# Kernel optimization log

Measured on AMD Instinct MI355X. Metric: run time of the kernel, lower is better.

## Reference

```python
import jax, jax.numpy as jnp
import numpy as np

NW, NT, ND, D = 30000, 2000, 20000, 128
E = {'ww': 600000, 'wt': 300000, 'wd': 400000, 'td': 100000, 'tt': 40000}
ENDS = {'ww': (NW, NW), 'wt': (NW, NT), 'wd': (NW, ND), 'td': (NT, ND), 'tt': (NT, NT)}


def setup_inputs() -> dict:
    key = jax.random.key(0)
    ks = iter(jax.random.split(key, 64))
    nrm = lambda shape: jax.random.normal(next(ks), shape, dtype=jnp.float32)
    inp = {}
    inp['feat_word'] = nrm((NW, D))
    inp['feat_topic'] = nrm((NT, D))
    # 'effect' node data: ~half the topics are causal (nonzero effect)
    inp['effect'] = jax.random.randint(next(ks), (NT,), 0, 2).astype(jnp.float32)
    # independent Bernoulli(0.1) draws for the td and tt iterations
    inp['bern_td'] = (jax.random.uniform(next(ks), (NT,)) < 0.1).astype(jnp.float32)
    inp['bern_tt'] = (jax.random.uniform(next(ks), (NT,)) < 0.1).astype(jnp.float32)
    for et, (ns, nd) in ENDS.items():
        inp[f'src_{et}'] = jax.random.randint(next(ks), (E[et],), 0, ns, dtype=jnp.int32)
        inp[f'dst_{et}'] = jax.random.randint(next(ks), (E[et],), 0, nd, dtype=jnp.int32)
        inp[f'w_{et}'] = jax.random.uniform(next(ks), (E[et],), dtype=jnp.float32)
    for name in ['ww', 'wt', 'wd', 'td', 'tt']:
        inp[f'W_{name}'] = nrm((D, D)) * 0.05
        inp[f'b_{name}'] = jnp.zeros((D,), jnp.float32)
    inp['W_causal'] = nrm((D, D)) * 0.05
    inp['W_noise'] = nrm((D, D)) * 0.05
    inp['n_doc'] = ND
    return inp


def _mean_agg(Wh, w, src, dst, n_dst):
    # DGL fn.u_mul_e + fn.mean: mean of (Wh[src]*w) over incoming edges; 0 for isolated dst
    m = Wh[src] * w[:, None]                                    # [E, D]
    s = jax.ops.segment_sum(m, dst, num_segments=n_dst)          # [n_dst, D]
    deg = jax.ops.segment_sum(jnp.ones_like(w), dst, num_segments=n_dst)
    return jnp.where(deg[:, None] > 0, s / jnp.maximum(deg, 1.0)[:, None], 0.0)


def reference(feat_word, feat_topic, effect, bern_td, bern_tt,
              src_ww, dst_ww, w_ww, src_wt, dst_wt, w_wt,
              src_wd, dst_wd, w_wd, src_td, dst_td, w_td,
              src_tt, dst_tt, w_tt,
              W_ww, b_ww, W_wt, b_wt, W_wd, b_wd, W_td, b_td, W_tt, b_tt,
              W_causal, W_noise, n_doc):
    n_word, n_topic = feat_word.shape[0], feat_topic.shape[0]
    # Phase 1: word -> word (ww)
    h_word = _mean_agg(feat_word @ W_ww + b_ww, w_ww, src_ww, dst_ww, n_word)
    # Phase 2: remaining etypes; word features replaced by h
    causal = (effect != 0).astype(feat_topic.dtype)[:, None]     # [NT, 1]
    rm_td = (bern_td * (effect == 0))[:, None]
    rm_tt = (bern_tt * (effect == 0))[:, None]
    Wh_wt = h_word @ W_wt + b_wt
    Wh_wd = h_word @ W_wd + b_wd
    Wh_td = (feat_topic @ W_td + b_td
             + (feat_topic * causal) @ W_causal - (feat_topic * rm_td) @ W_noise)
    Wh_tt = (feat_topic @ W_tt + b_tt
             + (feat_topic * causal) @ W_causal - (feat_topic * rm_tt) @ W_noise)
    # cross-relation 'sum' reducer per destination ntype
    h_topic = (_mean_agg(Wh_wt, w_wt, src_wt, dst_wt, n_topic)
               + _mean_agg(Wh_tt, w_tt, src_tt, dst_tt, n_topic))
    h_doc = (_mean_agg(Wh_wd, w_wd, src_wd, dst_wd, n_doc)
             + _mean_agg(Wh_td, w_td, src_td, dst_td, n_doc))
    return h_word, h_topic, h_doc
```

## Files before the change

### kernel.cpp

```cpp
#include <hip/hip_runtime.h>

#define D 128
typedef unsigned short u16;
constexpr int NW = 30000;
constexpr int NT = 2000;
constexpr int NDOC = 20000;

constexpr int CAPB = 1024;
constexpr int SSP  = 136;
constexpr int NBK_WW = (NW + 31) / 32;
constexpr int NBK_WT = NT / 4;
constexpr int NBK_TT = (NT + 31) / 32;
constexpr int NBK_WD = (NDOC + 31) / 32;
constexpr int NBK_TD = (NDOC + 31) / 32;
constexpr int BUK_WW = 0;
constexpr int BUK_WT = BUK_WW + NBK_WW;
constexpr int BUK_TT = BUK_WT + NBK_WT;
constexpr int BUK_WD = BUK_TT + NBK_TT;
constexpr int BUK_TD = BUK_WD + NBK_WD;
constexpr int NBUK   = BUK_TD + NBK_TD;

constexpr int EPB  = 4096;
constexpr int NF2B = (NW * D / 4 + 255) / 256;
constexpr int NMM4C = 32 * 4;
constexpr int NWTR  = 3 * 4;
constexpr int U3 = NBK_WW + NBK_TT + NBK_TD;
constexpr int U4 = NBK_WT + NBK_WD;

struct RelDesc { const int* src; const int* dst; const float* w;
                 int e0; int buk0; int shift; int mask; };
struct Rels { RelDesc r[5]; };

__device__ __forceinline__ int which_rel(const Rels& R, int e)
{
    if (e < R.r[1].e0) return 0;
    if (e < R.r[2].e0) return 1;
    if (e < R.r[3].e0) return 2;
    if (e < R.r[4].e0) return 3;
    return 4;
}

__device__ __forceinline__ float b2f(u16 h)
{
    return __uint_as_float(((unsigned)h) << 16);
}
__device__ __forceinline__ u16 f2b(float f)
{
    unsigned u = __float_as_uint(f);
    return (u16)((u + 0x7FFF + ((u >> 16) & 1)) >> 16);
}

typedef short bf16x8 __attribute__((ext_vector_type(8)));
typedef float f32x4 __attribute__((ext_vector_type(4)));
constexpr int WPITCH = 136;

struct BucketSmem {
    int2 st[CAPB];
    u16  Ssum[32 * SSP];
    float degL[32];
    float wsumL[32];
    int h2[32], exc[32], cnt[32];
};
struct PartSm { int hist[NBUK]; int baseL[NBUK]; };
union K1Sm {
    PartSm pt;
    u16 Wts[32 * WPITCH];
};

struct FP {
    const float *feat_word, *feat_topic;
    const float *effect, *bern_td, *bern_tt;
    Rels R;
    int Etot, npb;
    const float *W_td, *W_tt, *W_c, *W_n;
    const float *W_ww, *W_wt, *W_wd;
    const float *b_ww, *b_wt, *b_wd, *b_td, *b_tt;
    int* cur; int2* edataP;
    u16 *fw16, *hw16, *wtd16, *wtt16;
    u16 *Wtg_ww, *Wtg_wt, *Wtg_wd;
    u16* Sb2; float* degf2;
    float *h_word, *h_topic, *h_doc;
};

__device__ __forceinline__ void mm_slice(
    const float* __restrict__ Wg, int cs, u16* Wts, int tid)
{
    for (int i = tid; i < 32 * D; i += 256) {
        int k = i >> 5, nl = i & 31;
        Wts[nl * WPITCH + k] = f2b(Wg[k * D + cs * 32 + nl]);
    }
}

__device__ __forceinline__ void mm_acc2(
    const bf16x8 a[4], const u16* Wts, int lanelo, int quad, f32x4 acc[2])
{
#pragma unroll
    for (int c = 0; c < 2; ++c) {
        acc[c][0] = 0.f; acc[c][1] = 0.f; acc[c][2] = 0.f; acc[c][3] = 0.f;
    }
#pragma unroll
    for (int k0 = 0; k0 < 4; ++k0) {
#pragma unroll
        for (int c = 0; c < 2; ++c) {
            bf16x8 b = *(const bf16x8*)&Wts[(c * 16 + lanelo) * WPITCH
                                            + k0 * 32 + quad * 8];
            acc[c] = __builtin_amdgcn_mfma_f32_16x16x32_bf16(a[k0], b, acc[c], 0, 0, 0);
        }
    }
}

__device__ __forceinline__ void reduce_one_lds(
    const u16* __restrict__ Xb, const int2* st,
    int start, int end, int dl, int lane, BucketSmem& s)
{
    int half = lane >> 5;
    int q = (lane & 31) * 4;
    float4 acc = make_float4(0.f, 0.f, 0.f, 0.f);
    float wacc = 0.f;
    int j = start;
    for (; j + 32 <= end; j += 32) {
        int2 ee[16];
        ushort4 vv[16];
#pragma unroll
        for (int t = 0; t < 16; ++t) ee[t] = st[j + 2 * t + half];
#pragma unroll
        for (int t = 0; t < 16; ++t)
            vv[t] = *(const ushort4*)(Xb + (size_t)(ee[t].x & 0x7FFF) * D + q);
#pragma unroll
        for (int t = 0; t < 16; ++t) {
            float w = __int_as_float(ee[t].y);
            acc.x = fmaf(w, b2f(vv[t].x), acc.x);
            acc.y = fmaf(w, b2f(vv[t].y), acc.y);
            acc.z = fmaf(w, b2f(vv[t].z), acc.z);
            acc.w = fmaf(w, b2f(vv[t].w), acc.w);
            wacc += w;
        }
    }
    if (j + 16 <= end) {
        int2 ee[8];
        ushort4 vv[8];
#pragma unroll
        for (int t = 0; t < 8; ++t) ee[t] = st[j + 2 * t + half];
#pragma unroll
        for (int t = 0; t < 8; ++t)
            vv[t] = *(const ushort4*)(Xb + (size_t)(ee[t].x & 0x7FFF) * D + q);
#pragma unroll
        for (int t = 0; t < 8; ++t) {
            float w = __int_as_float(ee[t].y);
            acc.x = fmaf(w, b2f(vv[t].x), acc.x);
            acc.y = fmaf(w, b2f(vv[t].y), acc.y);
            acc.z = fmaf(w, b2f(vv[t].z), acc.z);
            acc.w = fmaf(w, b2f(vv[t].w), acc.w);
            wacc += w;
        }
        j += 16;
    }
    if (j + 8 <= end) {
        int2 ee[4];
        ushort4 vv[4];
#pragma unroll
        for (int t = 0; t < 4; ++t) ee[t] = st[j + 2 * t + half];
#pragma unroll
        for (int t = 0; t < 4; ++t)
            vv[t] = *(const ushort4*)(Xb + (size_t)(ee[t].x & 0x7FFF) * D + q);
#pragma unroll
        for (int t = 0; t < 4; ++t) {
            float w = __int_as_float(ee[t].y);
            acc.x = fmaf(w, b2f(vv[t].x), acc.x);
            acc.y = fmaf(w, b2f(vv[t].y), acc.y);
            acc.z = fmaf(w, b2f(vv[t].z), acc.z);
            acc.w = fmaf(w, b2f(vv[t].w), acc.w);
            wacc += w;
        }
        j += 8;
    }
    if (j + 4 <= end) {
        int2 ea = st[j + half];
        int2 eb = st[j + 2 + half];
        ushort4 va = *(const ushort4*)(Xb + (size_t)(ea.x & 0x7FFF) * D + q);
        ushort4 vb = *(const ushort4*)(Xb + (size_t)(eb.x & 0x7FFF) * D + q);
        float wa = __int_as_float(ea.y);
        float wb = __int_as_float(eb.y);
        acc.x = fmaf(wa, b2f(va.x), acc.x); acc.y = fmaf(wa, b2f(va.y), acc.y);
        acc.z = fmaf(wa, b2f(va.z), acc.z); acc.w = fmaf(wa, b2f(va.w), acc.w);
        acc.x = fmaf(wb, b2f(vb.x), acc.x); acc.y = fmaf(wb, b2f(vb.y), acc.y);
        acc.z = fmaf(wb, b2f(vb.z), acc.z); acc.w = fmaf(wb, b2f(vb.w), acc.w);
        wacc += wa + wb;
        j += 4;
    }
    for (; j < end; j += 2) {
        int jj = j + half;
        int2 e = st[jj < end ? jj : (end - 1)];
        float w = (jj < end) ? __int_as_float(e.y) : 0.f;
        ushort4 v = *(const ushort4*)(Xb + (size_t)(e.x & 0x7FFF) * D + q);
        acc.x = fmaf(w, b2f(v.x), acc.x); acc.y = fmaf(w, b2f(v.y), acc.y);
        acc.z = fmaf(w, b2f(v.z), acc.z); acc.w = fmaf(w, b2f(v.w), acc.w);
        wacc += w;
    }
    acc.x += __shfl_xor(acc.x, 32);
    acc.y += __shfl_xor(acc.y, 32);
    acc.z += __shfl_xor(acc.z, 32);
    acc.w += __shfl_xor(acc.w, 32);
    wacc  += __shfl_xor(wacc, 32);
    if (half == 0) {
        ushort4 o;
        o.x = f2b(acc.x); o.y = f2b(acc.y); o.z = f2b(acc.z); o.w = f2b(acc.w);
        *(ushort4*)(s.Ssum + dl * SSP + q) = o;
    }
    if (lane == 0) {
        s.degL[dl] = (float)(end - start);
        s.wsumL[dl] = wacc;
    }
}

__device__ __forceinline__ void bucket_reduce(
    const u16* __restrict__ X, const int* __restrict__ cur,
    const int2* __restrict__ edataP, int buk, int nsl, BucketSmem& s)
{
    int tid = threadIdx.x;
    int nE = min(cur[buk], CAPB);
    const int2* gsrc = edataP + (size_t)buk * CAPB;
    int2 ev[CAPB / 256];
#pragma unroll
    for (int t = 0; t < CAPB / 256; ++t) {
        int i = t * 256 + tid;
        if (i < nE) ev[t] = gsrc[i];
    }
    if (tid < 32) { s.h2[tid] = 0; s.cnt[tid] = 0; }
    __syncthreads();
#pragma unroll
    for (int t = 0; t < CAPB / 256; ++t) {
        int i = t * 256 + tid;
        if (i < nE) atomicAdd(&s.h2[(ev[t].x >> 15) & 31], 1);
    }
    __syncthreads();
    if (tid < 32) s.exc[tid] = s.h2[tid];
    __syncthreads();
    for (int off = 1; off < 32; off <<= 1) {
        int t = 0;
        if (tid < 32 && tid >= off) t = s.exc[tid - off];
        __syncthreads();
        if (tid < 32) s.exc[tid] += t;
        __syncthreads();
    }
    if (tid < 32) s.exc[tid] -= s.h2[tid];
    __syncthreads();
#pragma unroll
    for (int t = 0; t < CAPB / 256; ++t) {
        int i = t * 256 + tid;
        if (i < nE) {
            int dl = (ev[t].x >> 15) & 31;
            int rk = atomicAdd(&s.cnt[dl], 1);
            s.st[s.exc[dl] + rk] = ev[t];
        }
    }
    __syncthreads();
    int wv = tid >> 6, lane = tid & 63;
    for (int dl = wv; dl < nsl; dl += 4) {
        int start = s.exc[dl];
        reduce_one_lds(X, s.st, start, start + s.h2[dl], dl, lane, s);
    }
}

__device__ __forceinline__ void fused_mm(
    BucketSmem& s, const u16* __restrict__ Wtg, const float* __restrict__ bias,
    const u16* __restrict__ Tg, const float* __restrict__ degTg,
    float* __restrict__ Y, u16* __restrict__ Yb, int row0, int n, int tid)
{
    int wv = tid >> 6, lane = tid & 63;
    int lanelo = lane & 15, quad = lane >> 4;
    int rt = wv >> 1, ch = wv & 1;
    int arow = rt * 16 + lanelo;
    f32x4 acc[4];
#pragma unroll
    for (int c = 0; c < 4; ++c) {
        acc[c][0] = 0.f; acc[c][1] = 0.f; acc[c][2] = 0.f; acc[c][3] = 0.f;
    }
#pragma unroll
    for (int k0 = 0; k0 < 4; ++k0) {
        bf16x8 a;
        if (arow < n) {
            a = *(const bf16x8*)(s.Ssum + arow * SSP + k0 * 32 + quad * 8);
        } else {
#pragma unroll
            for (int j = 0; j < 8; ++j) a[j] = 0;
        }
#pragma unroll
        for (int c = 0; c < 4; ++c) {
            int ct = ch * 4 + c;
            bf16x8 b = *(const bf16x8*)(Wtg + (ct * 16 + lanelo) * D
                                        + k0 * 32 + quad * 8);
            acc[c] = __builtin_amdgcn_mfma_f32_16x16x32_bf16(a, b, acc[c], 0, 0, 0);
        }
    }
    int rbase = rt * 16 + quad * 4;
#pragma unroll
    for (int r = 0; r < 4; ++r) {
        int row = rbase + r;
        if (row >= n) continue;
        float dgv = s.degL[row];
        float wsv = s.wsumL[row];
        float dtv = degTg ? degTg[row] : 0.f;
#pragma unroll
        for (int c = 0; c < 4; ++c) {
            int ct = ch * 4 + c;
            int col = ct * 16 + lanelo;
            float y = acc[c][r];
            y = dgv > 0.f ? (y + wsv * bias[col]) / dgv : 0.f;
            if (Tg && dtv > 0.f) y += b2f(Tg[(size_t)row * D + col]) / dtv;
            Y[(size_t)(row0 + row) * D + col] = y;
            if (Yb) Yb[(size_t)(row0 + row) * D + col] = f2b(y);
        }
    }
}

__device__ __forceinline__ void dump_smem(
    BucketSmem& s, u16* __restrict__ Sg, float* __restrict__ degg,
    int nsl, int tid)
{
    for (int i = tid; i < nsl * 32; i += 256) {
        int row = i >> 5, c4 = (i & 31) * 4;
        *(ushort4*)(Sg + (size_t)row * D + c4) =
            *(const ushort4*)(s.Ssum + row * SSP + c4);
    }
    if (tid < nsl) degg[tid] = s.degL[tid];
}

__global__ __launch_bounds__(256) void prep_part_kernel(FP p)
{
    __shared__ K1Sm sm;
    int tid = threadIdx.x;
    int u = (int)blockIdx.x;

    if (u < p.npb) {
        for (int i = tid; i < NBUK; i += 256) sm.pt.hist[i] = 0;
        __syncthreads();
        int base_e = u * EPB;
        int bs[EPB / 256];
        int2 se[EPB / 256];
#pragma unroll
        for (int r = 0; r < EPB / 256; ++r) {
            int e = base_e + r * 256 + tid;
            if (e < p.Etot) {
                int k = which_rel(p.R, e);
                int le = e - p.R.r[k].e0;
                int s = p.R.r[k].src[le];
                int dd = p.R.r[k].dst[le];
                float w = p.R.r[k].w[le];
                int b = p.R.r[k].buk0 + (dd >> p.R.r[k].shift);
                int dloc = dd & p.R.r[k].mask;
                bs[r] = b;
                se[r] = make_int2(s | (dloc << 15), __float_as_int(w));
                atomicAdd(&sm.pt.hist[b], 1);
            } else {
                bs[r] = -1;
            }
        }
        __syncthreads();
        for (int i = tid; i < NBUK; i += 256)
            sm.pt.baseL[i] = sm.pt.hist[i]
                ? atomicAdd(&p.cur[i], sm.pt.hist[i]) : 0;
        __syncthreads();
        for (int i = tid; i < NBUK; i += 256) sm.pt.hist[i] = 0;
        __syncthreads();
#pragma unroll
        for (int r = 0; r < EPB / 256; ++r) {
            int b = bs[r];
            if (b >= 0) {
                int rk = atomicAdd(&sm.pt.hist[b], 1) + sm.pt.baseL[b];
                if (rk < CAPB)
                    p.edataP[(size_t)b * CAPB + rk] = se[r];
            }
        }
    } else if (u < p.npb + NF2B) {
        int i = (u - p.npb) * 256 + tid;
        if (i < NW * D / 4) {
            float4 v = ((const float4*)p.feat_word)[i];
            ushort4 o;
            o.x = f2b(v.x); o.y = f2b(v.y); o.z = f2b(v.z); o.w = f2b(v.w);
            ((ushort4*)p.fw16)[i] = o;
        }
    } else if (u < p.npb + NF2B + NMM4C) {
        int idx = u - p.npb - NF2B;
        int rt = idx >> 2, cs = idx & 3;
        int wv = tid >> 6, lane = tid & 63;
        int lanelo = lane & 15, quad = lane >> 4;
        int arow = rt * 64 + wv * 16 + lanelo;
        bf16x8 a[4];
#pragma unroll
        for (int k0 = 0; k0 < 4; ++k0) {
            if (arow < NT) {
                const float* ap = p.feat_topic + (size_t)arow * D
                                  + k0 * 32 + quad * 8;
                float4 a0 = *(const float4*)ap;
                float4 a1 = *(const float4*)(ap + 4);
                a[k0][0] = (short)f2b(a0.x); a[k0][1] = (short)f2b(a0.y);
                a[k0][2] = (short)f2b(a0.z); a[k0][3] = (short)f2b(a0.w);
                a[k0][4] = (short)f2b(a1.x); a[k0][5] = (short)f2b(a1.y);
                a[k0][6] = (short)f2b(a1.z); a[k0][7] = (short)f2b(a1.w);
            } else {
#pragma unroll
                for (int j = 0; j < 8; ++j) a[k0][j] = 0;
            }
        }
        f32x4 aC[2], aN[2], aM[2];
        mm_slice(p.W_c, cs, sm.Wts, tid);  __syncthreads();
        mm_acc2(a, sm.Wts, lanelo, quad, aC); __syncthreads();
        mm_slice(p.W_n, cs, sm.Wts, tid);  __syncthreads();
        mm_acc2(a, sm.Wts, lanelo, quad, aN); __syncthreads();

        int rbase = rt * 64 + wv * 16 + quad * 4;
#pragma unroll
        for (int m = 0; m < 2; ++m) {
            const float* Wg   = m == 0 ? p.W_td : p.W_tt;
            const float* bias = m == 0 ? p.b_td : p.b_tt;
            const float* bern = m == 0 ? p.bern_td : p.bern_tt;
            u16* out = m == 0 ? p.wtd16 : p.wtt16;
            mm_slice(Wg, cs, sm.Wts, tid); __syncthreads();
            mm_acc2(a, sm.Wts, lanelo, quad, aM);
            float b0 = bias[cs * 32 + lanelo];
            float b1 = bias[cs * 32 + 16 + lanelo];
#pragma unroll
            for (int r = 0; r < 4; ++r) {
                int row = rbase + r;
                if (row >= NT) continue;
                float eff = p.effect[row];
                float causal = (eff != 0.f) ? 1.f : 0.f;
                float zero = (eff == 0.f) ? 1.f : 0.f;
                float rm = bern[row] * zero;
                float v0 = aM[0][r] + b0 + causal * aC[0][r] - rm * aN[0][r];
                float v1 = aM[1][r] + b1 + causal * aC[1][r] - rm * aN[1][r];
                out[(size_t)row * D + cs * 32 + lanelo] = f2b(v0);
                out[(size_t)row * D + cs * 32 + 16 + lanelo] = f2b(v1);
            }
            __syncthreads();
        }
    } else {
        int idx = u - p.npb - NF2B - NMM4C;
        int which = idx >> 2, cs = idx & 3;
        const float* Wg = which == 0 ? p.W_ww : which == 1 ? p.W_wt : p.W_wd;
        u16* Wd = which == 0 ? p.Wtg_ww : which == 1 ? p.Wtg_wt : p.Wtg_wd;
        mm_slice(Wg, cs, sm.Wts, tid);
        __syncthreads();
        for (int i = tid; i < 32 * D; i += 256) {
            int nl = i >> 7, k = i & 127;
            Wd[(size_t)(cs * 32 + nl) * D + k] = sm.Wts[nl * WPITCH + k];
        }
    }
}

__global__ __launch_bounds__(256, 4) void phaseA_kernel(FP p)
{
    __shared__ BucketSmem bs;
    int u = (int)blockIdx.x;
    int tid = threadIdx.x;
    if (u < NBK_WW) {
        int w0 = u * 32;
        int nsl = min(32, NW - w0);
        bucket_reduce(p.fw16, p.cur, p.edataP, BUK_WW + u, nsl, bs);
        __syncthreads();
        fused_mm(bs, p.Wtg_ww, p.b_ww, nullptr, nullptr,
                 p.h_word, p.hw16, w0, nsl, tid);
    } else if (u < NBK_WW + NBK_TT) {
        int i = u - NBK_WW;
        int t0 = i * 32;
        int nsl = min(32, NT - t0);
        bucket_reduce(p.wtt16, p.cur, p.edataP, BUK_TT + i, nsl, bs);
        __syncthreads();
        dump_smem(bs, p.Sb2 + (size_t)t0 * D, p.degf2 + t0, nsl, tid);
    } else {
        int i = u - NBK_WW - NBK_TT;
        int d0 = i * 32;
        int nsl = min(32, NDOC - d0);
        bucket_reduce(p.wtd16, p.cur, p.edataP, BUK_TD + i, nsl, bs);
        __syncthreads();
        dump_smem(bs, p.Sb2 + (size_t)(NT + d0) * D, p.degf2 + NT + d0, nsl, tid);
    }
}

__global__ __launch_bounds__(256, 4) void phaseB_kernel(FP p)
{
    __shared__ BucketSmem bs;
    int u = (int)blockIdx.x;
    int tid = threadIdx.x;
    if (u < NBK_WT) {
        int t0 = u * 4;
        bucket_reduce(p.hw16, p.cur, p.edataP, BUK_WT + u, 4, bs);
        __syncthreads();
        fused_mm(bs, p.Wtg_wt, p.b_wt, p.Sb2 + (size_t)t0 * D,
                 p.degf2 + t0, p.h_topic, nullptr, t0, 4, tid);
    } else {
        int i = u - NBK_WT;
        int d0 = i * 32;
        int nsl = min(32, NDOC - d0);
        bucket_reduce(p.hw16, p.cur, p.edataP, BUK_WD + i, nsl, bs);
        __syncthreads();
        fused_mm(bs, p.Wtg_wd, p.b_wd, p.Sb2 + (size_t)(NT + d0) * D,
                 p.degf2 + NT + d0, p.h_doc, nullptr, d0, nsl, tid);
    }
}

extern "C" void kernel_launch(void* const* d_in, const int* in_sizes, int n_in,
                              void* d_out, int out_size, void* d_ws, size_t ws_size,
                              hipStream_t stream)
{
    const float* feat_word  = (const float*)d_in[0];
    const float* feat_topic = (const float*)d_in[1];
    const float* effect     = (const float*)d_in[2];
    const float* bern_td    = (const float*)d_in[3];
    const float* bern_tt    = (const float*)d_in[4];
    const int*   src_ww = (const int*)d_in[5];
    const int*   dst_ww = (const int*)d_in[6];
    const float* w_ww   = (const float*)d_in[7];
    const int*   src_wt = (const int*)d_in[8];
    const int*   dst_wt = (const int*)d_in[9];
    const float* w_wt   = (const float*)d_in[10];
    const int*   src_wd = (const int*)d_in[11];
    const int*   dst_wd = (const int*)d_in[12];
    const float* w_wd   = (const float*)d_in[13];
    const int*   src_td = (const int*)d_in[14];
    const int*   dst_td = (const int*)d_in[15];
    const float* w_td   = (const float*)d_in[16];
    const int*   src_tt = (const int*)d_in[17];
    const int*   dst_tt = (const int*)d_in[18];
    const float* w_tt   = (const float*)d_in[19];
    const float* W_ww = (const float*)d_in[20];
    const float* b_ww = (const float*)d_in[21];
    const float* W_wt = (const float*)d_in[22];
    const float* b_wt = (const float*)d_in[23];
    const float* W_wd = (const float*)d_in[24];
    const float* b_wd = (const float*)d_in[25];
    const float* W_td = (const float*)d_in[26];
    const float* b_td = (const float*)d_in[27];
    const float* W_tt = (const float*)d_in[28];
    const float* b_tt = (const float*)d_in[29];
    const float* W_causal = (const float*)d_in[30];
    const float* W_noise  = (const float*)d_in[31];

    const int E_ww = in_sizes[5];
    const int E_wt = in_sizes[8];
    const int E_wd = in_sizes[11];
    const int E_td = in_sizes[14];
    const int E_tt = in_sizes[17];
    const int E_total = E_ww + E_wt + E_wd + E_td + E_tt;

    float* ws = (float*)d_ws;
    u16*   Sb2   = (u16*)ws; ws += (long long)(NT + NDOC) * D / 2;
    float* degf2 = ws; ws += NT + NDOC;
    int*   cur   = (int*)ws; ws += NBUK;
    ws += ((size_t)(ws - (float*)d_ws) & 1);
    int2*  edataP = (int2*)ws; ws += (long long)2 * NBUK * CAPB;
    u16*   fw16  = (u16*)ws;  ws += (long long)NW * D / 2;
    u16*   hw16  = (u16*)ws;  ws += (long long)NW * D / 2;
    u16*   wtd16 = (u16*)ws;  ws += (long long)NT * D / 2;
    u16*   wtt16 = (u16*)ws;  ws += (long long)NT * D / 2;
    u16*   Wtg_ww = (u16*)ws; ws += (long long)D * D / 2;
    u16*   Wtg_wt = (u16*)ws; ws += (long long)D * D / 2;
    u16*   Wtg_wd = (u16*)ws; ws += (long long)D * D / 2;

    float* h_word  = (float*)d_out;
    float* h_topic = h_word + (long long)NW * D;
    float* h_doc   = h_topic + (long long)NT * D;

    FP p;
    p.feat_word = feat_word; p.feat_topic = feat_topic;
    p.effect = effect; p.bern_td = bern_td; p.bern_tt = bern_tt;
    p.R.r[0] = { src_ww, dst_ww, w_ww, 0,                         BUK_WW, 5, 31 };
    p.R.r[1] = { src_wt, dst_wt, w_wt, E_ww,                      BUK_WT, 2, 3  };
    p.R.r[2] = { src_tt, dst_tt, w_tt, E_ww + E_wt,               BUK_TT, 5, 31 };
    p.R.r[3] = { src_wd, dst_wd, w_wd, E_ww + E_wt + E_tt,        BUK_WD, 5, 31 };
    p.R.r[4] = { src_td, dst_td, w_td, E_ww + E_wt + E_tt + E_wd, BUK_TD, 5, 31 };
    p.Etot = E_total;
    p.npb = (E_total + EPB - 1) / EPB;
    p.W_td = W_td; p.W_tt = W_tt; p.W_c = W_causal; p.W_n = W_noise;
    p.W_ww = W_ww; p.W_wt = W_wt; p.W_wd = W_wd;
    p.b_ww = b_ww; p.b_wt = b_wt; p.b_wd = b_wd; p.b_td = b_td; p.b_tt = b_tt;
    p.cur = cur; p.edataP = edataP;
    p.fw16 = fw16; p.hw16 = hw16; p.wtd16 = wtd16; p.wtt16 = wtt16;
    p.Wtg_ww = Wtg_ww; p.Wtg_wt = Wtg_wt; p.Wtg_wd = Wtg_wd;
    p.Sb2 = Sb2; p.degf2 = degf2;
    p.h_word = h_word; p.h_topic = h_topic; p.h_doc = h_doc;

    hipMemsetAsync(cur, 0, NBUK * sizeof(int), stream);

    unsigned g1 = (unsigned)(p.npb + NF2B + NMM4C + NWTR);
    prep_part_kernel<<<g1, 256, 0, stream>>>(p);

    phaseA_kernel<<<U3, 256, 0, stream>>>(p);

    phaseB_kernel<<<U4, 256, 0, stream>>>(p);

    (void)n_in; (void)in_sizes; (void)out_size; (void)ws_size;
}
```

Baseline: 246.2 us.

## Split each destination bucket across two blocks handling half the rows

Each 32-destination bucket is now processed by two blocks, each reducing and multiplying only 16 destination rows, with the block index remapped so both halves of a bucket run in adjacent groups of 8. Shared memory for the partial sums shrinks to 16 rows and the fused MFMA matmul is reshaped so each wave handles two 16-column tiles of a single 16-row tile. The goal is more blocks and smaller per-block LDS, giving more parallelism and occupancy across the GPU. The cost is that both blocks load, histogram and sort the full bucket edge list, duplicating that work.

```diff
diff --git a/kernel.cpp b/kernel.cpp
--- a/kernel.cpp
+++ b/kernel.cpp
@@ -26,6 +26,8 @@
 constexpr int NWTR  = 3 * 4;
 constexpr int U3 = NBK_WW + NBK_TT + NBK_TD;
 constexpr int U4 = NBK_WT + NBK_WD;
+constexpr int GA = ((U3 + 7) / 8) * 16;
+constexpr int GB = ((U4 + 7) / 8) * 16;
 
 struct RelDesc { const int* src; const int* dst; const float* w;
                  int e0; int buk0; int shift; int mask; };
@@ -56,9 +58,9 @@
 
 struct BucketSmem {
     int2 st[CAPB];
-    u16  Ssum[32 * SSP];
-    float degL[32];
-    float wsumL[32];
+    u16  Ssum[16 * SSP];
+    float degL[16];
+    float wsumL[16];
     int h2[32], exc[32], cnt[32];
 };
 struct PartSm { int hist[NBUK]; int baseL[NBUK]; };
@@ -213,9 +215,9 @@
     }
 }
 
-__device__ __forceinline__ void bucket_reduce(
+__device__ __forceinline__ void bucket_reduce_half(
     const u16* __restrict__ X, const int* __restrict__ cur,
-    const int2* __restrict__ edataP, int buk, int nsl, BucketSmem& s)
+    const int2* __restrict__ edataP, int buk, int dl0, int nslh, BucketSmem& s)
 {
     int tid = threadIdx.x;
     int nE = min(cur[buk], CAPB);
@@ -256,44 +258,43 @@
     }
     __syncthreads();
     int wv = tid >> 6, lane = tid & 63;
-    for (int dl = wv; dl < nsl; dl += 4) {
+    for (int dll = wv; dll < nslh; dll += 4) {
+        int dl = dl0 + dll;
         int start = s.exc[dl];
-        reduce_one_lds(X, s.st, start, start + s.h2[dl], dl, lane, s);
-    }
-}
-
-__device__ __forceinline__ void fused_mm(
+        reduce_one_lds(X, s.st, start, start + s.h2[dl], dll, lane, s);
+    }
+}
+
+__device__ __forceinline__ void fused_mm16(
     BucketSmem& s, const u16* __restrict__ Wtg, const float* __restrict__ bias,
     const u16* __restrict__ Tg, const float* __restrict__ degTg,
-    float* __restrict__ Y, u16* __restrict__ Yb, int row0, int n, int tid)
+    float* __restrict__ Y, u16* __restrict__ Yb, long long row0, int n, int tid)
 {
     int wv = tid >> 6, lane = tid & 63;
     int lanelo = lane & 15, quad = lane >> 4;
-    int rt = wv >> 1, ch = wv & 1;
-    int arow = rt * 16 + lanelo;
-    f32x4 acc[4];
-#pragma unroll
-    for (int c = 0; c < 4; ++c) {
+    f32x4 acc[2];
+#pragma unroll
+    for (int c = 0; c < 2; ++c) {
         acc[c][0] = 0.f; acc[c][1] = 0.f; acc[c][2] = 0.f; acc[c][3] = 0.f;
     }
 #pragma unroll
     for (int k0 = 0; k0 < 4; ++k0) {
         bf16x8 a;
-        if (arow < n) {
-            a = *(const bf16x8*)(s.Ssum + arow * SSP + k0 * 32 + quad * 8);
+        if (lanelo < n) {
+            a = *(const bf16x8*)(s.Ssum + lanelo * SSP + k0 * 32 + quad * 8);
         } else {
 #pragma unroll
             for (int j = 0; j < 8; ++j) a[j] = 0;
         }
 #pragma unroll
-        for (int c = 0; c < 4; ++c) {
-            int ct = ch * 4 + c;
+        for (int c = 0; c < 2; ++c) {
+            int ct = wv * 2 + c;
             bf16x8 b = *(const bf16x8*)(Wtg + (ct * 16 + lanelo) * D
                                         + k0 * 32 + quad * 8);
             acc[c] = __builtin_amdgcn_mfma_f32_16x16x32_bf16(a, b, acc[c], 0, 0, 0);
         }
     }
-    int rbase = rt * 16 + quad * 4;
+    int rbase = quad * 4;
 #pragma unroll
     for (int r = 0; r < 4; ++r) {
         int row = rbase + r;
@@ -302,19 +303,19 @@
         float wsv = s.wsumL[row];
         float dtv = degTg ? degTg[row] : 0.f;
 #pragma unroll
-        for (int c = 0; c < 4; ++c) {
-            int ct = ch * 4 + c;
+        for (int c = 0; c < 2; ++c) {
+            int ct = wv * 2 + c;
             int col = ct * 16 + lanelo;
             float y = acc[c][r];
             y = dgv > 0.f ? (y + wsv * bias[col]) / dgv : 0.f;
             if (Tg && dtv > 0.f) y += b2f(Tg[(size_t)row * D + col]) / dtv;
-            Y[(size_t)(row0 + row) * D + col] = y;
-            if (Yb) Yb[(size_t)(row0 + row) * D + col] = f2b(y);
-        }
-    }
-}
-
-__device__ __forceinline__ void dump_smem(
+            Y[(row0 + row) * D + col] = y;
+            if (Yb) Yb[(row0 + row) * D + col] = f2b(y);
+        }
+    }
+}
+
+__device__ __forceinline__ void dump_smem16(
     BucketSmem& s, u16* __restrict__ Sg, float* __restrict__ degg,
     int nsl, int tid)
 {
@@ -452,51 +453,60 @@
 __global__ __launch_bounds__(256, 4) void phaseA_kernel(FP p)
 {
     __shared__ BucketSmem bs;
-    int u = (int)blockIdx.x;
+    int b = (int)blockIdx.x;
+    int u = ((b >> 4) << 3) | (b & 7);
+    int h = (b >> 3) & 1;
     int tid = threadIdx.x;
+    if (u >= U3) return;
     if (u < NBK_WW) {
-        int w0 = u * 32;
-        int nsl = min(32, NW - w0);
-        bucket_reduce(p.fw16, p.cur, p.edataP, BUK_WW + u, nsl, bs);
-        __syncthreads();
-        fused_mm(bs, p.Wtg_ww, p.b_ww, nullptr, nullptr,
-                 p.h_word, p.hw16, w0, nsl, tid);
+        long long w0 = (long long)u * 32 + h * 16;
+        int nslh = min(16, NW - (int)w0);
+        if (nslh <= 0) return;
+        bucket_reduce_half(p.fw16, p.cur, p.edataP, BUK_WW + u, h * 16, nslh, bs);
+        __syncthreads();
+        fused_mm16(bs, p.Wtg_ww, p.b_ww, nullptr, nullptr,
+                   p.h_word, p.hw16, w0, nslh, tid);
     } else if (u < NBK_WW + NBK_TT) {
         int i = u - NBK_WW;
-        int t0 = i * 32;
-        int nsl = min(32, NT - t0);
-        bucket_reduce(p.wtt16, p.cur, p.edataP, BUK_TT + i, nsl, bs);
-        __syncthreads();
-        dump_smem(bs, p.Sb2 + (size_t)t0 * D, p.degf2 + t0, nsl, tid);
+        int t0 = i * 32 + h * 16;
+        int nslh = min(16, NT - t0);
+        if (nslh <= 0) return;
+        bucket_reduce_half(p.wtt16, p.cur, p.edataP, BUK_TT + i, h * 16, nslh, bs);
+        __syncthreads();
+        dump_smem16(bs, p.Sb2 + (size_t)t0 * D, p.degf2 + t0, nslh, tid);
     } else {
         int i = u - NBK_WW - NBK_TT;
-        int d0 = i * 32;
-        int nsl = min(32, NDOC - d0);
-        bucket_reduce(p.wtd16, p.cur, p.edataP, BUK_TD + i, nsl, bs);
-        __syncthreads();
-        dump_smem(bs, p.Sb2 + (size_t)(NT + d0) * D, p.degf2 + NT + d0, nsl, tid);
+        int d0 = i * 32 + h * 16;
+        int nslh = min(16, NDOC - d0);
+        if (nslh <= 0) return;
+        bucket_reduce_half(p.wtd16, p.cur, p.edataP, BUK_TD + i, h * 16, nslh, bs);
+        __syncthreads();
+        dump_smem16(bs, p.Sb2 + (size_t)(NT + d0) * D, p.degf2 + NT + d0,
+                    nslh, tid);
     }
 }
 
 __global__ __launch_bounds__(256, 4) void phaseB_kernel(FP p)
 {
     __shared__ BucketSmem bs;
-    int u = (int)blockIdx.x;
+    int b = (int)blockIdx.x;
+    int u = ((b >> 4) << 3) | (b & 7);
+    int h = (b >> 3) & 1;
     int tid = threadIdx.x;
+    if (u >= U4) return;
     if (u < NBK_WT) {
-        int t0 = u * 4;
-        bucket_reduce(p.hw16, p.cur, p.edataP, BUK_WT + u, 4, bs);
-        __syncthreads();
-        fused_mm(bs, p.Wtg_wt, p.b_wt, p.Sb2 + (size_t)t0 * D,
-                 p.degf2 + t0, p.h_topic, nullptr, t0, 4, tid);
+        int t0 = u * 4 + h * 2;
+        bucket_reduce_half(p.hw16, p.cur, p.edataP, BUK_WT + u, h * 2, 2, bs);
+        __syncthreads();
+        fused_mm16(bs, p.Wtg_wt, p.b_wt, p.Sb2 + (size_t)t0 * D,
+                   p.degf2 + t0, p.h_topic, nullptr, t0, 2, tid);
     } else {
         int i = u - NBK_WT;
-        int d0 = i * 32;
-        int nsl = min(32, NDOC - d0);
-        bucket_reduce(p.hw16, p.cur, p.edataP, BUK_WD + i, nsl, bs);
-        __syncthreads();
-        fused_mm(bs, p.Wtg_wd, p.b_wd, p.Sb2 + (size_t)(NT + d0) * D,
-                 p.degf2 + NT + d0, p.h_doc, nullptr, d0, nsl, tid);
+        int d0 = i * 32 + h * 16;
+        bucket_reduce_half(p.hw16, p.cur, p.edataP, BUK_WD + i, h * 16, 16, bs);
+        __syncthreads();
+        fused_mm16(bs, p.Wtg_wd, p.b_wd, p.Sb2 + (size_t)(NT + d0) * D,
+                   p.degf2 + NT + d0, p.h_doc, nullptr, d0, 16, tid);
     }
 }
 
@@ -586,9 +596,9 @@
     unsigned g1 = (unsigned)(p.npb + NF2B + NMM4C + NWTR);
     prep_part_kernel<<<g1, 256, 0, stream>>>(p);
 
-    phaseA_kernel<<<U3, 256, 0, stream>>>(p);
-
-    phaseB_kernel<<<U4, 256, 0, stream>>>(p);
+    phaseA_kernel<<<GA, 256, 0, stream>>>(p);
+
+    phaseB_kernel<<<GB, 256, 0, stream>>>(p);
 
     (void)n_in; (void)in_sizes; (void)out_size; (void)ws_size;
 }
```

New measurement: 244.5 us. About the same (-0.7%).
